# Kernel tuning notes

Measured on AMD Instinct MI355X. Metric: run time of the kernel, lower is better.

## Reference

```python
import jax, jax.numpy as jnp
import numpy as np

B, T, C = 1, 2048, 1024
H, KVH = 16, 4
D = C // H            # 64
KV = KVH * D          # 256
EPS = 1e-6
SCALE = 1.0 / np.sqrt(D)
ROPE_BASE = 10000.0


def setup_inputs() -> dict:
    key = jax.random.key(0)
    ks = jax.random.split(key, 8)
    s = 0.02
    return dict(
        x=jax.random.normal(ks[0], (B, T, C), jnp.float32),
        Wq=jax.random.normal(ks[1], (C, C), jnp.float32) * s,
        Wk=jax.random.normal(ks[2], (KV, C), jnp.float32) * s,
        Wv=jax.random.normal(ks[3], (KV, C), jnp.float32) * s,
        Wo=jax.random.normal(ks[4], (C, C), jnp.float32) * s,
        q_norm_w=jnp.ones((C,), jnp.float32),
        k_norm_w=jnp.ones((KV,), jnp.float32),
        fgate_w=jax.random.normal(ks[5], (H, C), jnp.float32) * s,
        fgate_b=jnp.zeros((H,), jnp.float32),
        weight_lambda=jax.random.normal(ks[6], (C, H), jnp.float32) * s,
    )


def _rmsnorm(x, w):
    var = jnp.mean(x * x, axis=-1, keepdims=True)
    return x * jax.lax.rsqrt(var + EPS) * w


def _rotate_half(x):
    x1, x2 = jnp.split(x, 2, axis=-1)
    return jnp.concatenate([-x2, x1], axis=-1)


def _apply_rope(q, k):
    # q: [B,H,T,D], k: [B,KVH,T,D]; position_ids = arange(T)
    inv_freq = 1.0 / (ROPE_BASE ** (jnp.arange(0, D, 2, dtype=jnp.float32) / D))
    freqs = jnp.outer(jnp.arange(T, dtype=jnp.float32), inv_freq)  # [T, D/2]
    emb = jnp.concatenate([freqs, freqs], axis=-1)                 # [T, D]
    cos = jnp.cos(emb)[None, None]                                  # [1,1,T,D]
    sin = jnp.sin(emb)[None, None]
    return q * cos + _rotate_half(q) * sin, k * cos + _rotate_half(k) * sin


def _forward(x, Wq, Wk, Wv, Wo, q_norm_w, k_norm_w, fgate_w, fgate_b, weight_lambda):
    q = _rmsnorm(x @ Wq.T, q_norm_w)          # [B,T,C]
    k = _rmsnorm(x @ Wk.T, k_norm_w)          # [B,T,KV]
    v = x @ Wv.T                              # [B,T,KV]
    q = q.reshape(B, T, H, D).transpose(0, 2, 1, 3)     # [B,H,T,D]
    k = k.reshape(B, T, KVH, D).transpose(0, 2, 1, 3)   # [B,KVH,T,D]
    v = v.reshape(B, T, KVH, D).transpose(0, 2, 1, 3)
    q, k = _apply_rope(q, k)
    # GQA: repeat_interleave kv heads
    g = H // KVH
    k = jnp.repeat(k, g, axis=1)              # [B,H,T,D]
    v = jnp.repeat(v, g, axis=1)
    # Forgetting gate (FoX): log f_t per head, with elu-based lambda scaling
    lam = jax.nn.elu(x @ weight_lambda) + 1.0            # [B,T,H]
    logit = (x @ fgate_w.T + fgate_b) * lam              # [B,T,H]
    log_f = (jax.nn.log_sigmoid(logit) / (lam + 1e-3)).transpose(0, 2, 1)  # [B,H,T]
    c = jnp.cumsum(log_f, axis=-1)                       # [B,H,T]
    bias = c[..., :, None] - c[..., None, :]             # [B,H,T,T]: sum_{t=j+1..i} log f_t
    scores = jnp.einsum('bhid,bhjd->bhij', q, k) * SCALE + bias
    causal = jnp.tril(jnp.ones((T, T), dtype=bool))
    scores = jnp.where(causal, scores, -jnp.inf)
    p = jax.nn.softmax(scores, axis=-1)
    y = jnp.einsum('bhij,bhjd->bhid', p, v)              # [B,H,T,D]
    y = y.transpose(0, 2, 1, 3).reshape(B, T, C)
    return y @ Wo.T


def reference(x, Wq, Wk, Wv, Wo, q_norm_w, k_norm_w, fgate_w, fgate_b, weight_lambda):
    return _forward(x, Wq, Wk, Wv, Wo, q_norm_w, k_norm_w, fgate_w, fgate_b, weight_lambda)
```

## Files before the change

### kernel.cpp

```cpp
#include <hip/hip_runtime.h>

typedef __bf16 bf16x8 __attribute__((ext_vector_type(8)));
typedef float f32x4 __attribute__((ext_vector_type(4)));

#define MFMA_BF16 __builtin_amdgcn_mfma_f32_16x16x32_bf16

static constexpr int T_ = 2048;
static constexpr int C_ = 1024;
static constexpr int H_ = 16;
static constexpr int KVH_ = 4;
static constexpr int D_ = 64;
static constexpr float SCALE_ = 0.125f;
static constexpr float INVLN2_ = 1.4426950408889634f;
static constexpr float SCALE2_ = 0.125f * 1.4426950408889634f;
static constexpr float MSHIFT_ = 10.0f;

static constexpr int UPH_ = 528;
static constexpr int W_ = H_ * UPH_;
static constexpr int CHUNK_ = 8;
static constexpr int NBLK_ = W_ / CHUNK_;

__device__ inline void cvt8(__bf16* dst, const float* src) {
  float4 a = *(const float4*)src;
  float4 b = *(const float4*)(src + 4);
  bf16x8 r;
  r[0] = (__bf16)a.x; r[1] = (__bf16)a.y; r[2] = (__bf16)a.z; r[3] = (__bf16)a.w;
  r[4] = (__bf16)b.x; r[5] = (__bf16)b.y; r[6] = (__bf16)b.z; r[7] = (__bf16)b.w;
  *(bf16x8*)dst = r;
}

__global__ __launch_bounds__(256) void cvt_kernel(
    const float* __restrict__ x,  const float* __restrict__ wq,
    const float* __restrict__ wk, const float* __restrict__ wv,
    const float* __restrict__ wo, const float* __restrict__ wl,
    __bf16* __restrict__ xb,  __bf16* __restrict__ wqb,
    __bf16* __restrict__ wkb, __bf16* __restrict__ wvb,
    __bf16* __restrict__ wob, float* __restrict__ wlT,
    float* __restrict__ zbuf)
{
  size_t i8 = ((size_t)blockIdx.x * 256 + threadIdx.x) * 8;
  if (i8 < 2097152)       cvt8(xb  + i8,            x  + i8);
  else if (i8 < 3145728)  cvt8(wqb + (i8-2097152),  wq + (i8-2097152));
  else if (i8 < 3407872)  cvt8(wkb + (i8-3145728),  wk + (i8-3145728));
  else if (i8 < 3670016)  cvt8(wvb + (i8-3407872),  wv + (i8-3407872));
  else if (i8 < 4718592)  cvt8(wob + (i8-3670016),  wo + (i8-3670016));
  else if (i8 < 4734976) {
    size_t r = i8 - 4718592;
#pragma unroll
    for (int j = 0; j < 8; ++j) {
      size_t idx = r + j;
      size_t hh = idx >> 10, c = idx & 1023;
      wlT[idx] = wl[c * 16 + hh];
    }
  } else {
    size_t z = i8 - 4734976;
    if (z < 2129920) {
      float4 zz = {0.f, 0.f, 0.f, 0.f};
      *(float4*)(zbuf + z) = zz;
      *(float4*)(zbuf + z + 4) = zz;
    }
  }
}

template <int BM>
__global__ __launch_bounds__(256) void gemm_bt_kernel(
    const __bf16* __restrict__ A, int K, int N,
    const __bf16* __restrict__ B0, int e0,
    const __bf16* __restrict__ B1, int e1,
    const __bf16* __restrict__ B2,
    float* __restrict__ outF)
{
  __shared__ __bf16 la[BM * 40];
  __shared__ __bf16 lb[128 * 40];
  const int m0 = blockIdx.y * BM;
  const int n0 = blockIdx.x * 128;
  const __bf16* Bs; int nrel;
  if (n0 < e0)      { Bs = B0; nrel = n0; }
  else if (n0 < e1) { Bs = B1; nrel = n0 - e0; }
  else              { Bs = B2; nrel = n0 - e1; }
  const int tid = threadIdx.x;
  const int arow = tid >> 2, acol = (tid & 3) * 8;
  const __bf16* ap = A  + (size_t)(m0   + arow) * K + acol;
  const __bf16* bp = Bs + (size_t)(nrel + arow) * K + acol;
  const int w = tid >> 6, lane = tid & 63, lq = lane >> 4, ln = lane & 15;
  const int wm = (w >> 1) * (BM / 2), wn = (w & 1) * 64;
  constexpr int FM = BM / 32;
  f32x4 acc[FM][4] = {};
  for (int k0 = 0; k0 < K; k0 += 32) {
    bf16x8 a0 = *(const bf16x8*)(ap + k0);
    bf16x8 a1{};
    if (BM == 128) a1 = *(const bf16x8*)(ap + (size_t)64 * K + k0);
    bf16x8 b0 = *(const bf16x8*)(bp + k0);
    bf16x8 b1 = *(const bf16x8*)(bp + (size_t)64 * K + k0);
    __syncthreads();
    *(bf16x8*)(la + arow * 40 + acol) = a0;
    if (BM == 128) *(bf16x8*)(la + (arow + 64) * 40 + acol) = a1;
    *(bf16x8*)(lb + arow * 40 + acol) = b0;
    *(bf16x8*)(lb + (arow + 64) * 40 + acol) = b1;
    __syncthreads();
    bf16x8 af[FM], bfr[4];
#pragma unroll
    for (int i = 0; i < FM; ++i)
      af[i] = *(const bf16x8*)(la + (wm + i * 16 + ln) * 40 + lq * 8);
#pragma unroll
    for (int j = 0; j < 4; ++j)
      bfr[j] = *(const bf16x8*)(lb + (wn + j * 16 + ln) * 40 + lq * 8);
#pragma unroll
    for (int i = 0; i < FM; ++i)
#pragma unroll
      for (int j = 0; j < 4; ++j)
        acc[i][j] = MFMA_BF16(af[i], bfr[j], acc[i][j], 0, 0, 0);
  }
#pragma unroll
  for (int i = 0; i < FM; ++i)
#pragma unroll
    for (int j = 0; j < 4; ++j)
#pragma unroll
      for (int r = 0; r < 4; ++r) {
        int row = m0 + wm + i * 16 + lq * 4 + r;
        int col = n0 + wn + j * 16 + ln;
        outF[(size_t)row * N + col] = acc[i][j][r];
      }
}

__global__ __launch_bounds__(256) void gemmout_kernel(
    const float* __restrict__ oacc, const float* __restrict__ lsacc,
    const __bf16* __restrict__ B, float* __restrict__ outF)
{
  constexpr int K = 1024, N = 1024;
  __shared__ __bf16 la[64 * 40];
  __shared__ __bf16 lb[128 * 40];
  const int m0 = blockIdx.y * 64;
  const int n0 = blockIdx.x * 128;
  const int tid = threadIdx.x;
  const int arow = tid >> 2, acol = (tid & 3) * 8;
  const int trow = m0 + arow;
  const __bf16* bp = B + (size_t)(n0 + arow) * K + acol;
  const int w = tid >> 6, lane = tid & 63, lq = lane >> 4, ln = lane & 15;
  const int wm = (w >> 1) * 32, wn = (w & 1) * 64;
  f32x4 acc[2][4] = {};
  for (int k0 = 0; k0 < K; k0 += 32) {
    const int c = k0 + acol;
    const int hh = c >> 6, d = c & 63;
    const float* op = oacc + ((size_t)hh * T_ + trow) * D_ + d;
    float4 f0 = *(const float4*)(op);
    float4 f1 = *(const float4*)(op + 4);
    float inv = __builtin_amdgcn_rcpf(lsacc[(size_t)hh * T_ + trow]);
    bf16x8 a0;
    a0[0] = (__bf16)(f0.x * inv); a0[1] = (__bf16)(f0.y * inv);
    a0[2] = (__bf16)(f0.z * inv); a0[3] = (__bf16)(f0.w * inv);
    a0[4] = (__bf16)(f1.x * inv); a0[5] = (__bf16)(f1.y * inv);
    a0[6] = (__bf16)(f1.z * inv); a0[7] = (__bf16)(f1.w * inv);
    bf16x8 b0 = *(const bf16x8*)(bp + k0);
    bf16x8 b1 = *(const bf16x8*)(bp + (size_t)64 * K + k0);
    __syncthreads();
    *(bf16x8*)(la + arow * 40 + acol) = a0;
    *(bf16x8*)(lb + arow * 40 + acol) = b0;
    *(bf16x8*)(lb + (arow + 64) * 40 + acol) = b1;
    __syncthreads();
    bf16x8 af[2], bfr[4];
#pragma unroll
    for (int i = 0; i < 2; ++i)
      af[i] = *(const bf16x8*)(la + (wm + i * 16 + ln) * 40 + lq * 8);
#pragma unroll
    for (int j = 0; j < 4; ++j)
      bfr[j] = *(const bf16x8*)(lb + (wn + j * 16 + ln) * 40 + lq * 8);
#pragma unroll
    for (int i = 0; i < 2; ++i)
#pragma unroll
      for (int j = 0; j < 4; ++j)
        acc[i][j] = MFMA_BF16(af[i], bfr[j], acc[i][j], 0, 0, 0);
  }
#pragma unroll
  for (int i = 0; i < 2; ++i)
#pragma unroll
    for (int j = 0; j < 4; ++j)
#pragma unroll
      for (int r = 0; r < 4; ++r) {
        int row = m0 + wm + i * 16 + lq * 4 + r;
        int col = n0 + wn + j * 16 + ln;
        outF[(size_t)row * N + col] = acc[i][j][r];
      }
}

__global__ __launch_bounds__(256) void gates_kernel(
    const float* __restrict__ x, const float* __restrict__ fw,
    const float* __restrict__ fb, const float* __restrict__ wlT,
    float* __restrict__ logf)
{
  const int t = blockIdx.x;
  const int tid = threadIdx.x, w = tid >> 6, lane = tid & 63;
  float xv[16];
#pragma unroll
  for (int i = 0; i < 16; ++i)
    xv[i] = x[(size_t)t * C_ + i * 64 + lane];
#pragma unroll
  for (int u = 0; u < 4; ++u) {
    int h = w * 4 + u;
    float s1 = 0.f, s2 = 0.f;
#pragma unroll
    for (int i = 0; i < 16; ++i) {
      int cidx = i * 64 + lane;
      s1 += xv[i] * wlT[(size_t)h * C_ + cidx];
      s2 += xv[i] * fw[(size_t)h * C_ + cidx];
    }
    for (int m = 32; m; m >>= 1) {
      s1 += __shfl_xor(s1, m);
      s2 += __shfl_xor(s2, m);
    }
    if (lane == 0) {
      float lam = (s1 > 0.f ? s1 : expm1f(s1)) + 1.0f;
      float logit = (s2 + fb[h]) * lam;
      float ls = (logit >= 0.f) ? -log1pf(expf(-logit))
                                : (logit - log1pf(expf(logit)));
      logf[(size_t)h * T_ + t] = ls / (lam + 1e-3f);
    }
  }
}

__global__ __launch_bounds__(256) void cumsum_kernel(
    const float* __restrict__ logf, float* __restrict__ csum)
{
  const int h = blockIdx.x;
  const int tid = threadIdx.x, lane = tid & 63, w = tid >> 6;
  __shared__ float wsum[4];
  const float* src = logf + (size_t)h * T_ + tid * 8;
  float4 a = *(const float4*)(src);
  float4 b = *(const float4*)(src + 4);
  float v[8] = {a.x, a.y, a.z, a.w, b.x, b.y, b.z, b.w};
  float t = 0.f;
#pragma unroll
  for (int j = 0; j < 8; ++j) t += v[j];
  float s = t;
#pragma unroll
  for (int d = 1; d < 64; d <<= 1) {
    float u = __shfl_up(s, d);
    if (lane >= d) s += u;
  }
  if (lane == 63) wsum[w] = s;
  __syncthreads();
  float prefix = 0.f;
#pragma unroll
  for (int ww = 0; ww < 3; ++ww)
    if (ww < w) prefix += wsum[ww];
  float run = prefix + s - t;
  float* dst = csum + (size_t)h * T_ + tid * 8;
  float4 o0, o1;
  run += v[0]; o0.x = run; run += v[1]; o0.y = run;
  run += v[2]; o0.z = run; run += v[3]; o0.w = run;
  run += v[4]; o1.x = run; run += v[5]; o1.y = run;
  run += v[6]; o1.z = run; run += v[7]; o1.w = run;
  *(float4*)dst = o0;
  *(float4*)(dst + 4) = o1;
}

__global__ __launch_bounds__(256) void normrope_kernel(
    const float* __restrict__ qkv, const float* __restrict__ qw,
    const float* __restrict__ kw, __bf16* __restrict__ qh,
    __bf16* __restrict__ kh, __bf16* __restrict__ vh)
{
  const int t = blockIdx.x, tid = threadIdx.x;
  __shared__ float qn[1024];
  __shared__ float kn[256];
  __shared__ float red[16];
  __shared__ float rc[32], rs[32];
  if (tid < 32) {
    float fr = (float)t * exp2f((float)tid * -0.41524101186404527f);
    float sn, cs;
    sincosf(fr, &sn, &cs);
    rc[tid] = cs; rs[tid] = sn;
  }
  const float* row = qkv + (size_t)t * 1536;
  float4 q4 = *(const float4*)(row + tid * 4);
  float kvl = row[1024 + tid];
  float vvl = row[1280 + tid];
  float ssq = q4.x * q4.x + q4.y * q4.y + q4.z * q4.z + q4.w * q4.w;
  float ssk = kvl * kvl;
  const int lane = tid & 63, w = tid >> 6;
  for (int m = 32; m; m >>= 1) {
    ssq += __shfl_xor(ssq, m);
    ssk += __shfl_xor(ssk, m);
  }
  if (lane == 0) { red[w] = ssq; red[8 + w] = ssk; }
  __syncthreads();
  float sq = red[0] + red[1] + red[2] + red[3];
  float sk = red[8] + red[9] + red[10] + red[11];
  float rq = rsqrtf(sq * (1.0f / 1024.f) + 1e-6f);
  float rk = rsqrtf(sk * (1.0f / 256.f) + 1e-6f);
  qn[tid * 4 + 0] = q4.x * rq * qw[tid * 4 + 0];
  qn[tid * 4 + 1] = q4.y * rq * qw[tid * 4 + 1];
  qn[tid * 4 + 2] = q4.z * rq * qw[tid * 4 + 2];
  qn[tid * 4 + 3] = q4.w * rq * qw[tid * 4 + 3];
  kn[tid] = kvl * rk * kw[tid];
  __syncthreads();
#pragma unroll
  for (int u = 0; u < 4; ++u) {
    int cidx = tid * 4 + u;
    int hh = cidx >> 6, d = cidx & 63, i = d & 31;
    float cs = rc[i], sn = rs[i];
    float val = (d < 32) ? (qn[cidx] * cs - qn[cidx + 32] * sn)
                         : (qn[cidx] * cs + qn[cidx - 32] * sn);
    qh[(size_t)hh * T_ * D_ + (size_t)t * D_ + d] = (__bf16)val;
  }
  {
    int d = tid & 63, kvhh = tid >> 6, i = d & 31;
    float cs = rc[i], sn = rs[i];
    float kval = (d < 32) ? (kn[tid] * cs - kn[tid + 32] * sn)
                          : (kn[tid] * cs + kn[tid - 32] * sn);
    kh[(size_t)kvhh * T_ * D_ + (size_t)t * D_ + d] = (__bf16)kval;
    vh[(size_t)kvhh * T_ * D_ + (size_t)t * D_ + d] = (__bf16)vvl;
  }
}

__global__ __launch_bounds__(256) void vtrans_kernel(
    const __bf16* __restrict__ vh, __bf16* __restrict__ vt)
{
  const int tb = blockIdx.x, kvh = blockIdx.y;
  __shared__ __bf16 tile[64][72];
  const int tid = threadIdx.x;
  const int r = tid >> 2, cb = (tid & 3) * 16;
  const __bf16* src = vh + (size_t)kvh * T_ * D_ + (size_t)(tb * 64 + r) * D_ + cb;
  bf16x8 v0 = *(const bf16x8*)(src);
  bf16x8 v1 = *(const bf16x8*)(src + 8);
  *(bf16x8*)(&tile[r][cb]) = v0;
  *(bf16x8*)(&tile[r][cb + 8]) = v1;
  __syncthreads();
  bf16x8 o0, o1;
#pragma unroll
  for (int j = 0; j < 8; ++j) o0[j] = tile[cb + j][r];
#pragma unroll
  for (int j = 0; j < 8; ++j) o1[j] = tile[cb + 8 + j][r];
  __bf16* dst = vt + (size_t)kvh * D_ * T_ + (size_t)r * T_ + tb * 64 + cb;
  *(bf16x8*)(dst) = o0;
  *(bf16x8*)(dst + 8) = o1;
}

__global__ __launch_bounds__(256, 4) void attn_kernel(
    const __bf16* __restrict__ qh, const __bf16* __restrict__ kh,
    const __bf16* __restrict__ vt, const float* __restrict__ csum,
    float* __restrict__ oacc, float* __restrict__ lsacc)
{
  const int bid = blockIdx.x;
  const int wgid = (bid & 7) * (NBLK_ / 8) + (bid >> 3);
  const int u0 = wgid * CHUNK_;
  __shared__ __bf16 kbuf[2][64 * 72];
  __shared__ __bf16 vbuf[2][64 * 72];
  const int tid = threadIdx.x;
  const int w = tid >> 6, lane = tid & 63, lq = lane >> 4, ln = lane & 15;
  const int srow = tid >> 2, scol = (tid & 3) * 16;
  bf16x8 ones;
#pragma unroll
  for (int j = 0; j < 8; ++j) ones[j] = (__bf16)1.0f;

  auto dec = [](int u, int& h, int& ib, int& jt) {
    h = u / UPH_;
    int uh = u - h * UPH_;
    int b = (int)((sqrtf((float)(8 * uh + 1)) - 1.f) * 0.5f);
    if (b * (b + 1) / 2 > uh) --b;
    if ((b + 1) * (b + 2) / 2 <= uh) ++b;
    ib = b; jt = uh - b * (b + 1) / 2;
  };

  int h, ib, jt;
  dec(u0, h, ib, jt);
  int kvh = h >> 2;

  bf16x8 aq0, aq1;
  float ci2[4];
  f32x4 o[4] = {};
  f32x4 ls = {0.f, 0.f, 0.f, 0.f};
  auto loadQ = [&](int h_, int i0_) {
    const __bf16* qp = qh + ((size_t)h_ * T_ + i0_ + w * 16 + ln) * D_;
    aq0 = *(const bf16x8*)(qp + lq * 8);
    aq1 = *(const bf16x8*)(qp + 32 + lq * 8);
#pragma unroll
    for (int r = 0; r < 4; ++r)
      ci2[r] = (csum[(size_t)h_ * T_ + i0_ + w * 16 + lq * 4 + r] - MSHIFT_)
               * INVLN2_;
#pragma unroll
    for (int dd = 0; dd < 4; ++dd) o[dd] = f32x4{0.f, 0.f, 0.f, 0.f};
    ls = f32x4{0.f, 0.f, 0.f, 0.f};
  };
  loadQ(h, ib * 64);

  auto fetchRegs = [&](int kvh_, int jt_, bf16x8& k0, bf16x8& k1,
                       bf16x8& v0, bf16x8& v1) {
    const __bf16* kb = kh + (size_t)kvh_ * T_ * D_;
    const __bf16* vb = vt + (size_t)kvh_ * D_ * T_;
    k0 = *(const bf16x8*)(kb + (size_t)(jt_ * 64 + srow) * D_ + scol);
    k1 = *(const bf16x8*)(kb + (size_t)(jt_ * 64 + srow) * D_ + scol + 8);
    v0 = *(const bf16x8*)(vb + (size_t)srow * T_ + jt_ * 64 + scol);
    v1 = *(const bf16x8*)(vb + (size_t)srow * T_ + jt_ * 64 + scol + 8);
  };
  auto writeStage = [&](int cb, bf16x8 k0, bf16x8 k1, bf16x8 v0, bf16x8 v1) {
    *(bf16x8*)(kbuf[cb] + srow * 72 + scol) = k0;
    *(bf16x8*)(kbuf[cb] + srow * 72 + scol + 8) = k1;
    *(bf16x8*)(vbuf[cb] + srow * 72 + scol) = v0;
    *(bf16x8*)(vbuf[cb] + srow * 72 + scol + 8) = v1;
  };

  auto tilebody = [&](int cb, int j0, bool diag) {
    const __bf16* kt = kbuf[cb];
    const __bf16* vtt = vbuf[cb];
    __bf16* pw = kbuf[cb ^ 1] + w * 16 * 72;
    float cj2[4];
#pragma unroll
    for (int jj = 0; jj < 4; ++jj)
      cj2[jj] = csum[(size_t)h * T_ + j0 + jj * 16 + ln] * INVLN2_;
    f32x4 s[4];
    const f32x4 zf = {0.f, 0.f, 0.f, 0.f};
    __builtin_amdgcn_s_setprio(1);
#pragma unroll
    for (int jj = 0; jj < 4; ++jj) {
      bf16x8 bk0 = *(const bf16x8*)(kt + (jj * 16 + ln) * 72 + lq * 8);
      bf16x8 bk1 = *(const bf16x8*)(kt + (jj * 16 + ln) * 72 + 32 + lq * 8);
      s[jj] = MFMA_BF16(aq0, bk0, zf, 0, 0, 0);
      s[jj] = MFMA_BF16(aq1, bk1, s[jj], 0, 0, 0);
    }
    __builtin_amdgcn_s_setprio(0);
    bf16x8 bv0[4], bv1[4];
#pragma unroll
    for (int dd = 0; dd < 4; ++dd) {
      bv0[dd] = *(const bf16x8*)(vtt + (dd * 16 + ln) * 72 + lq * 8);
      bv1[dd] = *(const bf16x8*)(vtt + (dd * 16 + ln) * 72 + 32 + lq * 8);
    }
#pragma unroll
    for (int jj = 0; jj < 4; ++jj)
#pragma unroll
      for (int r = 0; r < 4; ++r) {
        float arg = fmaf(s[jj][r], SCALE2_, ci2[r] - cj2[jj]);
        float p = exp2f(arg);
        if (diag && (jj * 16 + ln > w * 16 + lq * 4 + r)) p = 0.f;
        pw[(lq * 4 + r) * 72 + jj * 16 + ln] = (__bf16)p;
      }
    asm volatile("s_waitcnt lgkmcnt(0)" ::: "memory");
    bf16x8 pa0 = *(const bf16x8*)(pw + ln * 72 + lq * 8);
    bf16x8 pa1 = *(const bf16x8*)(pw + ln * 72 + 32 + lq * 8);
    __builtin_amdgcn_s_setprio(1);
    ls = MFMA_BF16(pa0, ones, ls, 0, 0, 0);
    ls = MFMA_BF16(pa1, ones, ls, 0, 0, 0);
#pragma unroll
    for (int dd = 0; dd < 4; ++dd) {
      o[dd] = MFMA_BF16(pa0, bv0[dd], o[dd], 0, 0, 0);
      o[dd] = MFMA_BF16(pa1, bv1[dd], o[dd], 0, 0, 0);
    }
    __builtin_amdgcn_s_setprio(0);
  };

  auto flush = [&]() {
    const int i0 = ib * 64;
#pragma unroll
    for (int dd = 0; dd < 4; ++dd)
#pragma unroll
      for (int r = 0; r < 4; ++r) {
        int iabs = i0 + w * 16 + lq * 4 + r;
        atomicAdd(oacc + ((size_t)h * T_ + iabs) * D_ + dd * 16 + ln,
                  o[dd][r]);
      }
    if (ln == 0) {
#pragma unroll
      for (int r = 0; r < 4; ++r)
        atomicAdd(lsacc + (size_t)h * T_ + ib * 64 + w * 16 + lq * 4 + r,
                  ls[r]);
    }
  };

  {
    bf16x8 k0, k1, v0, v1;
    fetchRegs(kvh, jt, k0, k1, v0, v1);
    writeStage(0, k0, k1, v0, v1);
  }
  __syncthreads();

  int cur = 0;
#pragma unroll 1
  for (int s = 0; s < CHUNK_; ++s) {
    const bool last = (s == CHUNK_ - 1);
    int nh = 0, nib = 0, njt = 0;
    bf16x8 k0, k1, v0, v1;
    if (!last) {
      dec(u0 + s + 1, nh, nib, njt);
      fetchRegs(nh >> 2, njt, k0, k1, v0, v1);
    }
    tilebody(cur, jt * 64, jt == ib);
    if (!last) writeStage(cur ^ 1, k0, k1, v0, v1);
    const bool rowEnd = last || nib != ib || nh != h;
    if (rowEnd) flush();
    if (!last) {
      __syncthreads();
      if (nh != h || nib != ib) loadQ(nh, nib * 64);
      h = nh; ib = nib; jt = njt; kvh = nh >> 2;
      cur ^= 1;
    }
  }
}

extern "C" void kernel_launch(void* const* d_in, const int* in_sizes, int n_in,
                              void* d_out, int out_size, void* d_ws, size_t ws_size,
                              hipStream_t stream) {
  const float* x   = (const float*)d_in[0];
  const float* Wq  = (const float*)d_in[1];
  const float* Wk  = (const float*)d_in[2];
  const float* Wv  = (const float*)d_in[3];
  const float* Wo  = (const float*)d_in[4];
  const float* qnw = (const float*)d_in[5];
  const float* knw = (const float*)d_in[6];
  const float* fgw = (const float*)d_in[7];
  const float* fgb = (const float*)d_in[8];
  const float* wl  = (const float*)d_in[9];

  char* ws = (char*)d_ws;
  size_t off = 0;
  float*  qkv  = (float*)(ws + off);  off += (size_t)T_ * 1536 * 4;
  float*  logf = (float*)(ws + off);  off += (size_t)H_ * T_ * 4;
  float*  csum = (float*)(ws + off);  off += (size_t)H_ * T_ * 4;
  __bf16* qh   = (__bf16*)(ws + off); off += (size_t)H_ * T_ * D_ * 2;
  __bf16* kh   = (__bf16*)(ws + off); off += (size_t)KVH_ * T_ * D_ * 2;
  __bf16* vh   = (__bf16*)(ws + off); off += (size_t)KVH_ * T_ * D_ * 2;
  __bf16* vt   = (__bf16*)(ws + off); off += (size_t)KVH_ * T_ * D_ * 2;
  __bf16* xb   = (__bf16*)(ws + off); off += (size_t)T_ * C_ * 2;
  __bf16* wqb  = (__bf16*)(ws + off); off += (size_t)C_ * C_ * 2;
  __bf16* wkb  = (__bf16*)(ws + off); off += (size_t)256 * C_ * 2;
  __bf16* wvb  = (__bf16*)(ws + off); off += (size_t)256 * C_ * 2;
  __bf16* wob  = (__bf16*)(ws + off); off += (size_t)C_ * C_ * 2;
  float*  wlT  = (float*)(ws + off);  off += (size_t)H_ * C_ * 4;
  float*  oacc = (float*)(ws + off);  off += (size_t)H_ * T_ * D_ * 4;
  float*  lsacc= (float*)(ws + off);  off += (size_t)H_ * T_ * 4;

  cvt_kernel<<<3352, 256, 0, stream>>>(x, Wq, Wk, Wv, Wo, wl,
                                       xb, wqb, wkb, wvb, wob, wlT, oacc);
  gemm_bt_kernel<64><<<dim3(12, 32), 256, 0, stream>>>(
      xb, 1024, 1536, wqb, 1024, wkb, 1280, wvb, qkv);
  gates_kernel<<<T_, 256, 0, stream>>>(x, fgw, fgb, wlT, logf);
  cumsum_kernel<<<H_, 256, 0, stream>>>(logf, csum);
  normrope_kernel<<<T_, 256, 0, stream>>>(qkv, qnw, knw, qh, kh, vh);
  vtrans_kernel<<<dim3(T_ / 64, KVH_), 256, 0, stream>>>(vh, vt);
  attn_kernel<<<NBLK_, 256, 0, stream>>>(qh, kh, vt, csum, oacc, lsacc);
  gemmout_kernel<<<dim3(8, 32), 256, 0, stream>>>(
      oacc, lsacc, wob, (float*)d_out);
}
```

Baseline: 194.4 us.

## Transpose score MFMA, pack P writes, batch gate rows, retile GEMM and attention split

The attention kernel swaps the MFMA operands so each lane holds a score row, which allows vectorized csum loads and packed bf16 conversion with 8-byte LDS stores of P instead of scalar stores. The work split is rebalanced to 1024 blocks taking 9 or 8 tiles each. The gates kernel handles four timesteps per block so each weight load is reused across them, and the QKV GEMM moves to a 128-row tile with half as many blocks. Together these aim to cut LDS store traffic, redundant weight loads and launch overhead, with the risk of higher register pressure and uneven per-block work.

```diff
diff --git a/kernel.cpp b/kernel.cpp
--- a/kernel.cpp
+++ b/kernel.cpp
@@ -10,15 +10,12 @@
 static constexpr int H_ = 16;
 static constexpr int KVH_ = 4;
 static constexpr int D_ = 64;
-static constexpr float SCALE_ = 0.125f;
 static constexpr float INVLN2_ = 1.4426950408889634f;
 static constexpr float SCALE2_ = 0.125f * 1.4426950408889634f;
 static constexpr float MSHIFT_ = 10.0f;
 
 static constexpr int UPH_ = 528;
-static constexpr int W_ = H_ * UPH_;
-static constexpr int CHUNK_ = 8;
-static constexpr int NBLK_ = W_ / CHUNK_;
+static constexpr int NBLK_ = 1024;
 
 __device__ inline void cvt8(__bf16* dst, const float* src) {
   float4 a = *(const float4*)src;
@@ -188,32 +185,42 @@
     const float* __restrict__ fb, const float* __restrict__ wlT,
     float* __restrict__ logf)
 {
-  const int t = blockIdx.x;
+  const int t0 = blockIdx.x * 4;
   const int tid = threadIdx.x, w = tid >> 6, lane = tid & 63;
-  float xv[16];
-#pragma unroll
-  for (int i = 0; i < 16; ++i)
-    xv[i] = x[(size_t)t * C_ + i * 64 + lane];
+  float xv[4][16];
+#pragma unroll
+  for (int tt = 0; tt < 4; ++tt)
+#pragma unroll
+    for (int i = 0; i < 16; ++i)
+      xv[tt][i] = x[(size_t)(t0 + tt) * C_ + i * 64 + lane];
 #pragma unroll
   for (int u = 0; u < 4; ++u) {
     int h = w * 4 + u;
-    float s1 = 0.f, s2 = 0.f;
+    float wlr[16], fwr[16];
 #pragma unroll
     for (int i = 0; i < 16; ++i) {
-      int cidx = i * 64 + lane;
-      s1 += xv[i] * wlT[(size_t)h * C_ + cidx];
-      s2 += xv[i] * fw[(size_t)h * C_ + cidx];
-    }
-    for (int m = 32; m; m >>= 1) {
-      s1 += __shfl_xor(s1, m);
-      s2 += __shfl_xor(s2, m);
-    }
-    if (lane == 0) {
-      float lam = (s1 > 0.f ? s1 : expm1f(s1)) + 1.0f;
-      float logit = (s2 + fb[h]) * lam;
-      float ls = (logit >= 0.f) ? -log1pf(expf(-logit))
-                                : (logit - log1pf(expf(logit)));
-      logf[(size_t)h * T_ + t] = ls / (lam + 1e-3f);
+      wlr[i] = wlT[(size_t)h * C_ + i * 64 + lane];
+      fwr[i] = fw[(size_t)h * C_ + i * 64 + lane];
+    }
+#pragma unroll
+    for (int tt = 0; tt < 4; ++tt) {
+      float s1 = 0.f, s2 = 0.f;
+#pragma unroll
+      for (int i = 0; i < 16; ++i) {
+        s1 += xv[tt][i] * wlr[i];
+        s2 += xv[tt][i] * fwr[i];
+      }
+      for (int m = 32; m; m >>= 1) {
+        s1 += __shfl_xor(s1, m);
+        s2 += __shfl_xor(s2, m);
+      }
+      if (lane == 0) {
+        float lam = (s1 > 0.f ? s1 : expm1f(s1)) + 1.0f;
+        float logit = (s2 + fb[h]) * lam;
+        float ls = (logit >= 0.f) ? -log1pf(expf(-logit))
+                                  : (logit - log1pf(expf(logit)));
+        logf[(size_t)h * T_ + t0 + tt] = ls / (lam + 1e-3f);
+      }
     }
   }
 }
@@ -335,6 +342,12 @@
   *(bf16x8*)(dst + 8) = o1;
 }
 
+__device__ inline unsigned cvtpk_bf16(float a, float b) {
+  unsigned r;
+  asm("v_cvt_pk_bf16_f32 %0, %1, %2" : "=v"(r) : "v"(a), "v"(b));
+  return r;
+}
+
 __global__ __launch_bounds__(256, 4) void attn_kernel(
     const __bf16* __restrict__ qh, const __bf16* __restrict__ kh,
     const __bf16* __restrict__ vt, const float* __restrict__ csum,
@@ -342,7 +355,9 @@
 {
   const int bid = blockIdx.x;
   const int wgid = (bid & 7) * (NBLK_ / 8) + (bid >> 3);
-  const int u0 = wgid * CHUNK_;
+  const int g4 = wgid >> 2, r4 = wgid & 3;
+  const int u0 = g4 * 33 + (r4 ? 9 + (r4 - 1) * 8 : 0);
+  const int cnt = r4 ? 8 : 9;
   __shared__ __bf16 kbuf[2][64 * 72];
   __shared__ __bf16 vbuf[2][64 * 72];
   const int tid = threadIdx.x;
@@ -366,17 +381,14 @@
   int kvh = h >> 2;
 
   bf16x8 aq0, aq1;
-  float ci2[4];
+  float ci2;
   f32x4 o[4] = {};
   f32x4 ls = {0.f, 0.f, 0.f, 0.f};
   auto loadQ = [&](int h_, int i0_) {
     const __bf16* qp = qh + ((size_t)h_ * T_ + i0_ + w * 16 + ln) * D_;
     aq0 = *(const bf16x8*)(qp + lq * 8);
     aq1 = *(const bf16x8*)(qp + 32 + lq * 8);
-#pragma unroll
-    for (int r = 0; r < 4; ++r)
-      ci2[r] = (csum[(size_t)h_ * T_ + i0_ + w * 16 + lq * 4 + r] - MSHIFT_)
-               * INVLN2_;
+    ci2 = (csum[(size_t)h_ * T_ + i0_ + w * 16 + ln] - MSHIFT_) * INVLN2_;
 #pragma unroll
     for (int dd = 0; dd < 4; ++dd) o[dd] = f32x4{0.f, 0.f, 0.f, 0.f};
     ls = f32x4{0.f, 0.f, 0.f, 0.f};
@@ -403,10 +415,13 @@
     const __bf16* kt = kbuf[cb];
     const __bf16* vtt = vbuf[cb];
     __bf16* pw = kbuf[cb ^ 1] + w * 16 * 72;
-    float cj2[4];
-#pragma unroll
-    for (int jj = 0; jj < 4; ++jj)
-      cj2[jj] = csum[(size_t)h * T_ + j0 + jj * 16 + ln] * INVLN2_;
+    f32x4 cj2[4];
+#pragma unroll
+    for (int jj = 0; jj < 4; ++jj) {
+      float4 c4 = *(const float4*)(csum + (size_t)h * T_ + j0 + jj * 16 + lq * 4);
+      cj2[jj] = f32x4{c4.x * INVLN2_, c4.y * INVLN2_,
+                      c4.z * INVLN2_, c4.w * INVLN2_};
+    }
     f32x4 s[4];
     const f32x4 zf = {0.f, 0.f, 0.f, 0.f};
     __builtin_amdgcn_s_setprio(1);
@@ -414,8 +429,8 @@
     for (int jj = 0; jj < 4; ++jj) {
       bf16x8 bk0 = *(const bf16x8*)(kt + (jj * 16 + ln) * 72 + lq * 8);
       bf16x8 bk1 = *(const bf16x8*)(kt + (jj * 16 + ln) * 72 + 32 + lq * 8);
-      s[jj] = MFMA_BF16(aq0, bk0, zf, 0, 0, 0);
-      s[jj] = MFMA_BF16(aq1, bk1, s[jj], 0, 0, 0);
+      s[jj] = MFMA_BF16(bk0, aq0, zf, 0, 0, 0);
+      s[jj] = MFMA_BF16(bk1, aq1, s[jj], 0, 0, 0);
     }
     __builtin_amdgcn_s_setprio(0);
     bf16x8 bv0[4], bv1[4];
@@ -424,15 +439,21 @@
       bv0[dd] = *(const bf16x8*)(vtt + (dd * 16 + ln) * 72 + lq * 8);
       bv1[dd] = *(const bf16x8*)(vtt + (dd * 16 + ln) * 72 + 32 + lq * 8);
     }
-#pragma unroll
-    for (int jj = 0; jj < 4; ++jj)
+    const int qloc = w * 16 + ln;
+#pragma unroll
+    for (int jj = 0; jj < 4; ++jj) {
+      float p[4];
 #pragma unroll
       for (int r = 0; r < 4; ++r) {
-        float arg = fmaf(s[jj][r], SCALE2_, ci2[r] - cj2[jj]);
-        float p = exp2f(arg);
-        if (diag && (jj * 16 + ln > w * 16 + lq * 4 + r)) p = 0.f;
-        pw[(lq * 4 + r) * 72 + jj * 16 + ln] = (__bf16)p;
-      }
+        float arg = fmaf(s[jj][r], SCALE2_, ci2 - cj2[jj][r]);
+        p[r] = exp2f(arg);
+        if (diag && (jj * 16 + lq * 4 + r > qloc)) p[r] = 0.f;
+      }
+      unsigned lo = cvtpk_bf16(p[0], p[1]);
+      unsigned hi = cvtpk_bf16(p[2], p[3]);
+      uint2 pr; pr.x = lo; pr.y = hi;
+      *(uint2*)(pw + ln * 72 + jj * 16 + lq * 4) = pr;
+    }
     asm volatile("s_waitcnt lgkmcnt(0)" ::: "memory");
     bf16x8 pa0 = *(const bf16x8*)(pw + ln * 72 + lq * 8);
     bf16x8 pa1 = *(const bf16x8*)(pw + ln * 72 + 32 + lq * 8);
@@ -474,8 +495,8 @@
 
   int cur = 0;
 #pragma unroll 1
-  for (int s = 0; s < CHUNK_; ++s) {
-    const bool last = (s == CHUNK_ - 1);
+  for (int s = 0; s < cnt; ++s) {
+    const bool last = (s == cnt - 1);
     int nh = 0, nib = 0, njt = 0;
     bf16x8 k0, k1, v0, v1;
     if (!last) {
@@ -529,9 +550,9 @@
 
   cvt_kernel<<<3352, 256, 0, stream>>>(x, Wq, Wk, Wv, Wo, wl,
                                        xb, wqb, wkb, wvb, wob, wlT, oacc);
-  gemm_bt_kernel<64><<<dim3(12, 32), 256, 0, stream>>>(
+  gemm_bt_kernel<128><<<dim3(12, 16), 256, 0, stream>>>(
       xb, 1024, 1536, wqb, 1024, wkb, 1280, wvb, qkv);
-  gates_kernel<<<T_, 256, 0, stream>>>(x, fgw, fgb, wlT, logf);
+  gates_kernel<<<T_ / 4, 256, 0, stream>>>(x, fgw, fgb, wlT, logf);
   cumsum_kernel<<<H_, 256, 0, stream>>>(logf, csum);
   normrope_kernel<<<T_, 256, 0, stream>>>(qkv, qnw, knw, qh, kh, vh);
   vtrans_kernel<<<dim3(T_ / 64, KVH_), 256, 0, stream>>>(vh, vt);
```

Result: no change. 197.7 us (+1.7%).
